# Optimization experiments

Measured on AMD Instinct MI355X. Metric: run time of the kernel, lower is better.

Reference implementation:

```python
import jax, jax.numpy as jnp
import numpy as np

DMODEL = 1024
N_MAMBAS = 4
D_INNER = 2 * DMODEL          # expand = 2
D_STATE = 16                  # mamba_ssm default
D_CONV = 4                    # mamba_ssm default
DT_RANK = DMODEL // 16        # ceil(d_model/16) = 64


def setup_inputs() -> dict:
    key = jax.random.key(0)
    ks = jax.random.split(key, 8)
    B, L, n = 2, 4096, N_MAMBAS
    f32 = jnp.float32
    x = jax.random.normal(ks[0], (B, L, DMODEL), f32)
    in_w = jax.random.normal(ks[1], (n, 2 * D_INNER, DMODEL), f32) * 0.02
    conv_w = jax.random.normal(ks[2], (n, D_INNER, D_CONV), f32) * 0.1
    conv_b = jnp.zeros((n, D_INNER), f32)
    xproj_w = jax.random.normal(ks[3], (n, DT_RANK + 2 * D_STATE, D_INNER), f32) * 0.02
    dt_w = jax.random.normal(ks[4], (n, D_INNER, DT_RANK), f32) * 0.02
    # softplus-inverse of dt_init ~ 0.01 (mamba-style dt bias init)
    dt_b = jnp.log(jnp.expm1(jnp.full((n, D_INNER), 0.01, f32)))
    # S4D-real init: A_log = log(1..d_state)
    A_log = jnp.log(jnp.broadcast_to(jnp.arange(1, D_STATE + 1, dtype=f32), (n, D_INNER, D_STATE)))
    D_skip = jnp.ones((n, D_INNER), f32)
    out_w = jax.random.normal(ks[5], (n, DMODEL, D_INNER), f32) * 0.02
    return dict(x=x, in_w=in_w, conv_w=conv_w, conv_b=conv_b, xproj_w=xproj_w,
                dt_w=dt_w, dt_b=dt_b, A_log=A_log, D_skip=D_skip, out_w=out_w)


def _mamba(x, in_w, conv_w, conv_b, xproj_w, dt_w, dt_b, A_log, D_skip, out_w):
    # x: (B, Lc, D)
    Bb = x.shape[0]
    xz = jnp.einsum('bld,ed->ble', x, in_w)                 # (B, Lc, 2*D_INNER)
    xi, z = jnp.split(xz, 2, axis=-1)
    # causal depthwise conv over time
    xc = jnp.transpose(xi, (0, 2, 1))                       # (B, D_INNER, Lc)
    xc = jax.lax.conv_general_dilated(xc, conv_w[:, None, :], (1,),
                                      [(D_CONV - 1, 0)], feature_group_count=D_INNER)
    xi = jax.nn.silu(jnp.transpose(xc + conv_b[None, :, None], (0, 2, 1)))  # (B, Lc, D_INNER)
    proj = jnp.einsum('bld,ed->ble', xi, xproj_w)           # (B, Lc, DT_RANK + 2*D_STATE)
    dt = proj[..., :DT_RANK]
    Bm = proj[..., DT_RANK:DT_RANK + D_STATE]
    Cm = proj[..., DT_RANK + D_STATE:]
    dt = jax.nn.softplus(jnp.einsum('blr,dr->bld', dt, dt_w) + dt_b)  # (B, Lc, D_INNER)
    A = -jnp.exp(A_log)                                     # (D_INNER, D_STATE)

    def step(h, inp):
        dt_t, B_t, C_t, x_t = inp                           # (B,Di),(B,Ds),(B,Ds),(B,Di)
        dA = jnp.exp(dt_t[:, :, None] * A)                  # (B, Di, Ds)
        h = dA * h + dt_t[:, :, None] * B_t[:, None, :] * x_t[:, :, None]
        return h, jnp.einsum('bds,bs->bd', h, C_t)

    h0 = jnp.zeros((Bb, D_INNER, D_STATE), x.dtype)
    xs_t = (jnp.swapaxes(dt, 0, 1), jnp.swapaxes(Bm, 0, 1),
            jnp.swapaxes(Cm, 0, 1), jnp.swapaxes(xi, 0, 1))
    _, ys = jax.lax.scan(step, h0, xs_t)                    # (Lc, B, D_INNER)
    y = jnp.swapaxes(ys, 0, 1) + xi * D_skip                # (B, Lc, D_INNER)
    y = y * jax.nn.silu(z)
    return jnp.einsum('ble,de->bld', y, out_w)              # (B, Lc, D)


def reference(x, in_w, conv_w, conv_b, xproj_w, dt_w, dt_b, A_log, D_skip, out_w):
    B, L, D = x.shape
    n = N_MAMBAS
    # strided slices x[:, i::n] == reshape(B, L//n, n, D)[:, :, i]
    xs = jnp.transpose(x.reshape(B, L // n, n, D), (2, 0, 1, 3))   # (n, B, Lc, D)
    ys = jax.vmap(_mamba)(xs, in_w, conv_w, conv_b, xproj_w,
                          dt_w, dt_b, A_log, D_skip, out_w)        # (n, B, Lc, D)
    # torch.cat(dim=1) concatenates per-mamba outputs block-wise along seq
    return jnp.transpose(ys, (1, 0, 2, 3)).reshape(B, L, D)
```

## Files before the change

### kernel.cpp

```cpp
#include <hip/hip_runtime.h>
#include <math.h>

#define DM   1024
#define DI   2048
#define DSn  16
#define DTR  64
#define PW   96
#define LS   1024
#define NCH  16
#define CL   64
#define XKS  8

typedef unsigned short u16;
typedef unsigned int   u32;
typedef __attribute__((ext_vector_type(8))) short bf16x8;
typedef __attribute__((ext_vector_type(8))) unsigned short u16x8;
typedef __attribute__((ext_vector_type(4))) float f32x4;

__device__ __forceinline__ void bar_lds() {
  asm volatile("s_waitcnt lgkmcnt(0)\n\ts_barrier" ::: "memory");
}

__device__ __forceinline__ void split2(float f, u16& hi, u16& lo) {
  union { float f; unsigned int u; } v; v.f = f;
  hi = (u16)(v.u >> 16);
  union { unsigned int u; float f; } w; w.u = v.u & 0xffff0000u;
  union { float f; unsigned int u; } r; r.f = f - w.f;
  lo = (u16)(r.u >> 16);
}

template<int ROWS>
__device__ __forceinline__ bf16x8 frag(const u16* T, int l4, int row) {
  return *(const bf16x8*)&T[(l4 * ROWS + row) * 8];
}

template<int ROWS>
__device__ __forceinline__ void stage16f(const float* a, u16* Th, u16* Tl, int ra, int half) {
  #pragma unroll
  for (int q = 0; q < 2; ++q) {
    u16x8 vh, vl;
    #pragma unroll
    for (int c = 0; c < 8; ++c) {
      u16 h_, l_;
      split2(a[q * 8 + c], h_, l_);
      vh[c] = h_; vl[c] = l_;
    }
    const int slot = ((half * 2 + q) * ROWS + ra) * 8;
    *(u16x8*)&Th[slot] = vh;
    *(u16x8*)&Tl[slot] = vl;
  }
}

__global__ __launch_bounds__(256) void k_split_x(
    const float* __restrict__ x, u16* __restrict__ xh, u16* __restrict__ xl, int ib0)
{
  const int idx = blockIdx.x * 256 + threadIdx.x;
  const int t = idx >> 8, kq = (idx & 255) * 4;
  const int gt = ib0 * 1024 + t;
  const int j = gt & (LS - 1), ib = gt >> 10;
  const int i = ib >> 1, bb = ib & 1;
  const float4 v = *(const float4*)&x[(size_t)(bb * 4096 + j * 4 + i) * DM + kq];
  ushort4 vh, vl;
  split2(v.x, vh.x, vl.x); split2(v.y, vh.y, vl.y);
  split2(v.z, vh.z, vl.z); split2(v.w, vh.w, vl.w);
  *(ushort4*)&xh[(size_t)t * DM + kq] = vh;
  *(ushort4*)&xl[(size_t)t * DM + kq] = vl;
}

#define KGP 2064
__global__ __launch_bounds__(512, 2) void k_inproj(
    const u16* __restrict__ xh, const u16* __restrict__ xl,
    const float* __restrict__ inwf,
    float* __restrict__ xz, int ib0, int swz)
{
  __shared__ __align__(16) u16 L[2][4][4][KGP];
  const int tid = threadIdx.x;
  int mblk, nblk;
  if (swz) {
    const int o = blockIdx.x;
    const int xcd = o & 7, within = o >> 3;
    mblk = xcd * 4 + (within & 3);
    nblk = within >> 2;
  } else {
    mblk = blockIdx.x; nblk = blockIdx.y;
  }
  const int m0 = mblk << 8, n0 = nblk << 8;
  const int ib = ib0 + (m0 >> 10);
  const int il = (ib >> 1) - (ib0 >> 1);
  const int ra = tid >> 1, half = tid & 1;
  const u16* Aph = xh + (size_t)(m0 + ra) * DM + half * 16;
  const u16* Apl = xl + (size_t)(m0 + ra) * DM + half * 16;
  const float* Bpf = inwf + ((size_t)il * 4096 + n0 + ra) * DM + half * 16;
  const int w = tid >> 6, lane = tid & 63;
  const int wr = w >> 2, wc = w & 3;
  const int l15 = lane & 15, l4 = lane >> 4;

  f32x4 acc[8][4];
  #pragma unroll
  for (int a_ = 0; a_ < 8; ++a_)
    #pragma unroll
    for (int b_ = 0; b_ < 4; ++b_) acc[a_][b_] = (f32x4)(0.f);

  u16x8 ah2[2], al2[2];
  float br[16];

  auto LOADG = [&](int kt) {
    const int k0 = kt * 32;
    ah2[0] = *(const u16x8*)(Aph + k0);
    ah2[1] = *(const u16x8*)(Aph + k0 + 8);
    al2[0] = *(const u16x8*)(Apl + k0);
    al2[1] = *(const u16x8*)(Apl + k0 + 8);
    *(f32x4*)&br[0]  = *(const f32x4*)(Bpf + k0);
    *(f32x4*)&br[4]  = *(const f32x4*)(Bpf + k0 + 4);
    *(f32x4*)&br[8]  = *(const f32x4*)(Bpf + k0 + 8);
    *(f32x4*)&br[12] = *(const f32x4*)(Bpf + k0 + 12);
  };
  auto STORE = [&](int b) {
    #pragma unroll
    for (int q = 0; q < 2; ++q) {
      const int kg = half * 2 + q;
      *(u16x8*)&L[b][0][kg][ra * 8] = ah2[q];
      *(u16x8*)&L[b][1][kg][ra * 8] = al2[q];
      u16x8 vh, vl;
      #pragma unroll
      for (int c = 0; c < 8; ++c) {
        u16 h_, l_;
        split2(br[q * 8 + c], h_, l_);
        vh[c] = h_; vl[c] = l_;
      }
      *(u16x8*)&L[b][2][kg][ra * 8] = vh;
      *(u16x8*)&L[b][3][kg][ra * 8] = vl;
    }
  };
  auto COMPUTE = [&](int b) {
    bf16x8 bh[4], bl[4];
    #pragma unroll
    for (int nf = 0; nf < 4; ++nf) {
      const int col = wc * 64 + nf * 16 + l15;
      bh[nf] = *(const bf16x8*)&L[b][2][l4][col * 8];
      bl[nf] = *(const bf16x8*)&L[b][3][l4][col * 8];
    }
    #pragma unroll
    for (int mf = 0; mf < 8; ++mf) {
      const int row = wr * 128 + mf * 16 + l15;
      bf16x8 ah = *(const bf16x8*)&L[b][0][l4][row * 8];
      bf16x8 al = *(const bf16x8*)&L[b][1][l4][row * 8];
      #pragma unroll
      for (int nf = 0; nf < 4; ++nf) {
        acc[mf][nf] = __builtin_amdgcn_mfma_f32_16x16x32_bf16(ah, bh[nf], acc[mf][nf], 0, 0, 0);
        acc[mf][nf] = __builtin_amdgcn_mfma_f32_16x16x32_bf16(ah, bl[nf], acc[mf][nf], 0, 0, 0);
        acc[mf][nf] = __builtin_amdgcn_mfma_f32_16x16x32_bf16(al, bh[nf], acc[mf][nf], 0, 0, 0);
      }
    }
  };

  const int nk = DM / 32;
  LOADG(0);
  STORE(0);
  if (nk > 1) LOADG(1);
  bar_lds();
  for (int kt = 0; kt < nk; ++kt) {
    const int c = kt & 1;
    if (kt + 1 < nk) STORE(c ^ 1);
    if (kt + 2 < nk) LOADG(kt + 2);
    COMPUTE(c);
    bar_lds();
  }

  #pragma unroll
  for (int mf = 0; mf < 8; ++mf) {
    const int row = m0 + wr * 128 + mf * 16 + l4 * 4;
    #pragma unroll
    for (int nf = 0; nf < 4; ++nf) {
      const int col = n0 + wc * 64 + nf * 16 + l15;
      #pragma unroll
      for (int r = 0; r < 4; ++r)
        xz[(size_t)(row + r) * (2 * DI) + col] = acc[mf][nf][r];
    }
  }
}

__global__ __launch_bounds__(256) void k_conv(
    const float* __restrict__ xz, const float* __restrict__ convw,
    const float* __restrict__ convb, float* __restrict__ xib,
    int ib0, int ntok)
{
  const int idx = blockIdx.x * 256 + threadIdx.x;
  if (idx >= ntok * (DI / 4)) return;
  const int t = idx / (DI / 4);
  const int c = (idx - t * (DI / 4)) * 4;
  const int j = t & (LS - 1);
  const int i = (ib0 + (t >> 10)) >> 1;
  float4 acc = *(const float4*)&convb[(size_t)i * DI + c];
  float4 wt[4];
  #pragma unroll
  for (int q = 0; q < 4; ++q)
    wt[q] = *(const float4*)&convw[((size_t)i * DI + c + q) * 4];
  #pragma unroll
  for (int k = 0; k < 4; ++k) {
    const int j2 = j + k - 3;
    if (j2 >= 0) {
      const float4 v = *(const float4*)&xz[(size_t)(t + k - 3) * (2 * DI) + c];
      acc.x = fmaf(v.x, ((const float*)&wt[0])[k], acc.x);
      acc.y = fmaf(v.y, ((const float*)&wt[1])[k], acc.y);
      acc.z = fmaf(v.z, ((const float*)&wt[2])[k], acc.z);
      acc.w = fmaf(v.w, ((const float*)&wt[3])[k], acc.w);
    }
  }
  float4 o;
  o.x = acc.x / (1.f + __expf(-acc.x));
  o.y = acc.y / (1.f + __expf(-acc.y));
  o.z = acc.z / (1.f + __expf(-acc.z));
  o.w = acc.w / (1.f + __expf(-acc.w));
  *(float4*)&xib[(size_t)t * DI + c] = o;
}

__global__ __launch_bounds__(256) void k_xproj_part(
    const float* __restrict__ xif, const float* __restrict__ xwf,
    float* __restrict__ Pp, int ib0, int ntok)
{
  __shared__ __align__(16) u16 Ah[4*64*8], Al[4*64*8];
  __shared__ __align__(16) u16 Bh[4*96*8], Bl[4*96*8];
  const int tid = threadIdx.x;
  const int m0 = blockIdx.x << 6;
  const int ks = blockIdx.y;
  const int kbase = ks * (DI / XKS);
  const int ib = ib0 + (m0 >> 10);
  const int il = (ib >> 1) - (ib0 >> 1);
  const int ra = tid >> 1, half = tid & 1;
  const bool hasA = (tid < 128);
  const bool hasB = (tid < 192);
  const float* Apf = xif + (size_t)(m0 + ra) * DI + kbase + half * 16;
  const float* Bpf = xwf + ((size_t)il * PW + ra) * DI + kbase + half * 16;
  const int w = tid >> 6, lane = tid & 63;
  const int l15 = lane & 15, l4 = lane >> 4;

  f32x4 acc[6];
  #pragma unroll
  for (int b_ = 0; b_ < 6; ++b_) acc[b_] = (f32x4)(0.f);

  float ar[16], br[16];
  if (hasA) {
    #pragma unroll
    for (int q = 0; q < 4; ++q) *(f32x4*)&ar[q*4] = *(const f32x4*)(Apf + q*4);
  }
  if (hasB) {
    #pragma unroll
    for (int q = 0; q < 4; ++q) *(f32x4*)&br[q*4] = *(const f32x4*)(Bpf + q*4);
  }
  const int nk = (DI / XKS) / 32;
  for (int kt = 0; kt < nk; ++kt) {
    bar_lds();
    if (hasA) stage16f<64>(ar, Ah, Al, ra, half);
    if (hasB) stage16f<96>(br, Bh, Bl, ra, half);
    bar_lds();
    if (kt + 1 < nk) {
      const int k0 = (kt + 1) * 32;
      if (hasA) {
        #pragma unroll
        for (int q = 0; q < 4; ++q) *(f32x4*)&ar[q*4] = *(const f32x4*)(Apf + k0 + q*4);
      }
      if (hasB) {
        #pragma unroll
        for (int q = 0; q < 4; ++q) *(f32x4*)&br[q*4] = *(const f32x4*)(Bpf + k0 + q*4);
      }
    }
    const int arow = w * 16 + l15;
    bf16x8 ah = frag<64>(Ah, l4, arow);
    bf16x8 al = frag<64>(Al, l4, arow);
    #pragma unroll
    for (int nf = 0; nf < 6; ++nf) {
      const int col = nf * 16 + l15;
      bf16x8 bh = frag<96>(Bh, l4, col);
      bf16x8 bl = frag<96>(Bl, l4, col);
      acc[nf] = __builtin_amdgcn_mfma_f32_16x16x32_bf16(ah, bh, acc[nf], 0, 0, 0);
      acc[nf] = __builtin_amdgcn_mfma_f32_16x16x32_bf16(ah, bl, acc[nf], 0, 0, 0);
      acc[nf] = __builtin_amdgcn_mfma_f32_16x16x32_bf16(al, bh, acc[nf], 0, 0, 0);
    }
  }
  float* outp = Pp + (size_t)ks * ntok * PW;
  const int row = m0 + w * 16 + l4 * 4;
  #pragma unroll
  for (int nf = 0; nf < 6; ++nf) {
    const int col = nf * 16 + l15;
    #pragma unroll
    for (int r = 0; r < 4; ++r)
      outp[(size_t)(row + r) * PW + col] = acc[nf][r];
  }
}

__global__ __launch_bounds__(256) void k_xproj_red(
    const float* __restrict__ Pp, float* __restrict__ projb, int ntok)
{
  const int idx = blockIdx.x * 256 + threadIdx.x;
  if (idx >= ntok * PW) return;
  const size_t plane = (size_t)ntok * PW;
  float s = 0.f;
  #pragma unroll
  for (int ks = 0; ks < XKS; ++ks) s += Pp[(size_t)ks * plane + idx];
  projb[idx] = s;
}

__global__ __launch_bounds__(256) void k_dtproj(
    const float* __restrict__ proj, const float* __restrict__ dtw,
    const float* __restrict__ dtbias, float* __restrict__ dtout,
    int dstride, int ib0)
{
  __shared__ float As[16][132];
  __shared__ float Bs[16][132];
  const int tid = threadIdx.x;
  const int n0 = blockIdx.x << 7;
  const int m0 = blockIdx.y << 7;
  const int ib = ib0 + (m0 >> 10);
  const int i  = ib >> 1;
  const int ar = tid >> 2, kq = tid & 3;
  const float* A0 = proj + (size_t)(m0 + ar) * PW + kq * 4;
  const float* A1 = A0 + (size_t)64 * PW;
  const float* Wb = dtw + (size_t)i * DI * DTR;
  const float* B0 = Wb + (size_t)(n0 + ar) * DTR + kq * 4;
  const float* B1 = B0 + (size_t)64 * DTR;
  const int tx = tid & 15, ty = tid >> 4;
  float acc[8][8] = {};
  for (int kt = 0; kt < DTR / 16; ++kt) {
    const int k0 = kt * 16;
    float4 a0 = *(const float4*)(A0 + k0);
    float4 a1 = *(const float4*)(A1 + k0);
    float4 b0 = *(const float4*)(B0 + k0);
    float4 b1 = *(const float4*)(B1 + k0);
    __syncthreads();
    As[kq*4+0][ar] = a0.x; As[kq*4+1][ar] = a0.y; As[kq*4+2][ar] = a0.z; As[kq*4+3][ar] = a0.w;
    As[kq*4+0][ar+64] = a1.x; As[kq*4+1][ar+64] = a1.y; As[kq*4+2][ar+64] = a1.z; As[kq*4+3][ar+64] = a1.w;
    Bs[kq*4+0][ar] = b0.x; Bs[kq*4+1][ar] = b0.y; Bs[kq*4+2][ar] = b0.z; Bs[kq*4+3][ar] = b0.w;
    Bs[kq*4+0][ar+64] = b1.x; Bs[kq*4+1][ar+64] = b1.y; Bs[kq*4+2][ar+64] = b1.z; Bs[kq*4+3][ar+64] = b1.w;
    __syncthreads();
    #pragma unroll
    for (int k = 0; k < 16; ++k) {
      const float4 av0 = *(const float4*)&As[k][ty*8];
      const float4 av1 = *(const float4*)&As[k][ty*8+4];
      const float4 bv0 = *(const float4*)&Bs[k][tx*8];
      const float4 bv1 = *(const float4*)&Bs[k][tx*8+4];
      const float aa[8] = {av0.x,av0.y,av0.z,av0.w,av1.x,av1.y,av1.z,av1.w};
      const float bv[8] = {bv0.x,bv0.y,bv0.z,bv0.w,bv1.x,bv1.y,bv1.z,bv1.w};
      #pragma unroll
      for (int r = 0; r < 8; ++r)
        #pragma unroll
        for (int c = 0; c < 8; ++c)
          acc[r][c] = fmaf(aa[r], bv[c], acc[r][c]);
    }
  }
  float bias[8];
  #pragma unroll
  for (int c = 0; c < 8; ++c) bias[c] = dtbias[(size_t)i * DI + n0 + tx*8 + c];
  #pragma unroll
  for (int r = 0; r < 8; ++r) {
    const int t = m0 + ty*8 + r;
    #pragma unroll
    for (int c = 0; c < 8; ++c) {
      float u = acc[r][c] + bias[c];
      float sp = (u > 20.f) ? u : log1pf(__expf(u));
      dtout[(size_t)t * dstride + n0 + tx*8 + c] = sp;
    }
  }
}

__global__ __launch_bounds__(256) void k_scan_part(
    const float* __restrict__ projb, const float* dtp, int dstride,
    const float* __restrict__ xib, const float* __restrict__ A_log,
    float* __restrict__ Pbuf, float* __restrict__ Hbuf, int ib0)
{
  const int d = blockIdx.x * 256 + threadIdx.x;
  const int ch = blockIdx.y, lib = blockIdx.z;
  const int i = (ib0 + lib) >> 1;
  const size_t gd = (size_t)i * DI + d;
  __shared__ float bs[CL][DSn];
  const size_t trow = (size_t)lib * LS + (size_t)ch * CL;
  for (int p = threadIdx.x; p < CL * DSn; p += 256) {
    const int jj = p >> 4, ss = p & 15;
    bs[jj][ss] = projb[(trow + jj) * PW + DTR + ss];
  }
  float A[DSn], P[DSn], h[DSn];
  #pragma unroll
  for (int s = 0; s < DSn; ++s) {
    A[s] = -__expf(A_log[gd * DSn + s]);
    P[s] = 1.f; h[s] = 0.f;
  }
  __syncthreads();
  float dt_c = dtp[trow * dstride + d];
  float xi_c = xib[trow * DI + d];
  for (int j = 0; j < CL; ++j) {
    float dt_n = 0.f, xi_n = 0.f;
    if (j + 1 < CL) {
      dt_n = dtp[(trow + j + 1) * dstride + d];
      xi_n = xib[(trow + j + 1) * DI + d];
    }
    const float dx = dt_c * xi_c;
    #pragma unroll
    for (int s = 0; s < DSn; ++s) {
      const float dA = __expf(dt_c * A[s]);
      P[s] *= dA;
      h[s] = fmaf(dA, h[s], dx * bs[j][s]);
    }
    dt_c = dt_n; xi_c = xi_n;
  }
  const size_t base = ((size_t)(lib * NCH + ch) * DSn) * DI + d;
  #pragma unroll
  for (int s = 0; s < DSn; ++s) {
    Pbuf[base + (size_t)s * DI] = P[s];
    Hbuf[base + (size_t)s * DI] = h[s];
  }
}

__global__ __launch_bounds__(256) void k_scan_mid(
    float* __restrict__ Pbuf, const float* __restrict__ Hbuf, int nib)
{
  const int idx = blockIdx.x * 256 + threadIdx.x;
  if (idx >= nib * DSn * DI) return;
  const int d = idx & (DI - 1);
  const int s = (idx >> 11) & 15;
  const int lib = idx >> 15;
  const size_t stride = (size_t)DSn * DI;
  const size_t base = ((size_t)lib * NCH * DSn + s) * DI + d;
  float carry = 0.f;
  for (int c = 0; c < NCH; ++c) {
    const size_t o = base + (size_t)c * stride;
    const float p = Pbuf[o];
    const float hl = Hbuf[o];
    Pbuf[o] = carry;
    carry = fmaf(p, carry, hl);
  }
}

__global__ __launch_bounds__(256) void k_scan_full(
    const float* __restrict__ projb, const float* dtp, int dstride,
    float* xibio, const float* xzz,
    const float* __restrict__ A_log, const float* __restrict__ D_skip,
    const float* __restrict__ Pbuf, int ib0)
{
  const int d = blockIdx.x * 256 + threadIdx.x;
  const int ch = blockIdx.y, lib = blockIdx.z;
  const int i = (ib0 + lib) >> 1;
  const size_t gd = (size_t)i * DI + d;
  __shared__ float bs[CL][2 * DSn];
  const size_t trow = (size_t)lib * LS + (size_t)ch * CL;
  for (int p = threadIdx.x; p < CL * 2 * DSn; p += 256) {
    const int jj = p >> 5, ss = p & 31;
    bs[jj][ss] = projb[(trow + jj) * PW + DTR + ss];
  }
  float A[DSn], h[DSn];
  const size_t hbase = ((size_t)(lib * NCH + ch) * DSn) * DI + d;
  #pragma unroll
  for (int s = 0; s < DSn; ++s) {
    A[s] = -__expf(A_log[gd * DSn + s]);
    h[s] = Pbuf[hbase + (size_t)s * DI];
  }
  const float Dsk = D_skip[gd];
  __syncthreads();
  float dt_c = dtp[trow * dstride + d];
  float xi_c = xibio[trow * DI + d];
  float z_c  = xzz[trow * (2 * DI) + DI + d];
  for (int j = 0; j < CL; ++j) {
    float dt_n = 0.f, xi_n = 0.f, z_n = 0.f;
    if (j + 1 < CL) {
      dt_n = dtp[(trow + j + 1) * dstride + d];
      xi_n = xibio[(trow + j + 1) * DI + d];
      z_n  = xzz[(trow + j + 1) * (2 * DI) + DI + d];
    }
    const float dx = dt_c * xi_c;
    float y = 0.f;
    #pragma unroll
    for (int s = 0; s < DSn; ++s) {
      const float dA = __expf(dt_c * A[s]);
      h[s] = fmaf(dA, h[s], dx * bs[j][s]);
      y = fmaf(h[s], bs[j][DSn + s], y);
    }
    const float sz = z_c / (1.f + __expf(-z_c));
    const float val = (y + xi_c * Dsk) * sz;
    u16 vh, vl;
    split2(val, vh, vl);
    ((u32*)xibio)[(trow + j) * DI + d] = ((u32)vh << 16) | (u32)vl;
    dt_c = dt_n; xi_c = xi_n; z_c = z_n;
  }
}

__global__ __launch_bounds__(256) void k_outproj(
    const u32* __restrict__ ybp, const float* __restrict__ owf,
    float* __restrict__ out, int ib0)
{
  __shared__ __align__(16) u16 Ah[4*128*8], Al[4*128*8];
  __shared__ __align__(16) u16 Bh[4*128*8], Bl[4*128*8];
  const int tid = threadIdx.x;
  const int m0 = blockIdx.x << 7;
  const int n0 = blockIdx.y << 7;
  const int ib = ib0 + (m0 >> 10);
  const int i = ib >> 1, bb = ib & 1;
  const int il = i - (ib0 >> 1);
  const int ra = tid >> 1, half = tid & 1;
  const u32* Ap = ybp + (size_t)(m0 + ra) * DI + half * 16;
  const int rb = tid >> 1;
  const float* Bpf = owf + ((size_t)il * DM + n0 + rb) * DI + half * 16;
  const int w = tid >> 6, lane = tid & 63;
  const int wr = w >> 1, wc = w & 1;
  const int l15 = lane & 15, l4 = lane >> 4;

  f32x4 acc[4][4];
  #pragma unroll
  for (int a_ = 0; a_ < 4; ++a_)
    #pragma unroll
    for (int b_ = 0; b_ < 4; ++b_) acc[a_][b_] = (f32x4)(0.f);

  uint4 qa[4];
  float br[16];
  qa[0] = *(const uint4*)(Ap);     qa[1] = *(const uint4*)(Ap + 4);
  qa[2] = *(const uint4*)(Ap + 8); qa[3] = *(const uint4*)(Ap + 12);
  #pragma unroll
  for (int q = 0; q < 4; ++q) *(f32x4*)&br[q*4] = *(const f32x4*)(Bpf + q*4);
  const int nk = DI / 32;
  for (int kt = 0; kt < nk; ++kt) {
    bar_lds();
    #pragma unroll
    for (int g = 0; g < 2; ++g) {
      const u32 e[8] = { qa[2*g].x, qa[2*g].y, qa[2*g].z, qa[2*g].w,
                         qa[2*g+1].x, qa[2*g+1].y, qa[2*g+1].z, qa[2*g+1].w };
      u16x8 vh, vl;
      #pragma unroll
      for (int c = 0; c < 8; ++c) { vh[c] = (u16)(e[c] >> 16); vl[c] = (u16)(e[c] & 0xffffu); }
      const int slot = ((half*2+g)*128 + ra)*8;
      *(u16x8*)&Ah[slot] = vh;
      *(u16x8*)&Al[slot] = vl;
    }
    stage16f<128>(br, Bh, Bl, rb, half);
    bar_lds();
    if (kt + 1 < nk) {
      const int k0 = (kt + 1) * 32;
      qa[0] = *(const uint4*)(Ap + k0);     qa[1] = *(const uint4*)(Ap + k0 + 4);
      qa[2] = *(const uint4*)(Ap + k0 + 8); qa[3] = *(const uint4*)(Ap + k0 + 12);
      #pragma unroll
      for (int q = 0; q < 4; ++q) *(f32x4*)&br[q*4] = *(const f32x4*)(Bpf + k0 + q*4);
    }
    bf16x8 ah[4], al[4];
    #pragma unroll
    for (int mf = 0; mf < 4; ++mf) {
      const int row = wr * 64 + mf * 16 + l15;
      ah[mf] = frag<128>(Ah, l4, row);
      al[mf] = frag<128>(Al, l4, row);
    }
    #pragma unroll
    for (int nf = 0; nf < 4; ++nf) {
      const int col = wc * 64 + nf * 16 + l15;
      bf16x8 bh = frag<128>(Bh, l4, col);
      bf16x8 bl = frag<128>(Bl, l4, col);
      #pragma unroll
      for (int mf = 0; mf < 4; ++mf) {
        acc[mf][nf] = __builtin_amdgcn_mfma_f32_16x16x32_bf16(ah[mf], bh, acc[mf][nf], 0, 0, 0);
        acc[mf][nf] = __builtin_amdgcn_mfma_f32_16x16x32_bf16(ah[mf], bl, acc[mf][nf], 0, 0, 0);
        acc[mf][nf] = __builtin_amdgcn_mfma_f32_16x16x32_bf16(al[mf], bh, acc[mf][nf], 0, 0, 0);
      }
    }
  }
  #pragma unroll
  for (int mf = 0; mf < 4; ++mf) {
    const int t0 = m0 + wr * 64 + mf * 16 + l4 * 4;
    #pragma unroll
    for (int nf = 0; nf < 4; ++nf) {
      const int col = n0 + wc * 64 + nf * 16 + l15;
      #pragma unroll
      for (int r = 0; r < 4; ++r) {
        const int j = (t0 + r) & (LS - 1);
        out[(size_t)(bb * 4096 + i * 1024 + j) * DM + col] = acc[mf][nf][r];
      }
    }
  }
}

extern "C" void kernel_launch(void* const* d_in, const int* in_sizes, int n_in,
                              void* d_out, int out_size, void* d_ws, size_t ws_size,
                              hipStream_t stream) {
  (void)in_sizes; (void)n_in; (void)out_size;
  const float* x       = (const float*)d_in[0];
  const float* in_w    = (const float*)d_in[1];
  const float* conv_w  = (const float*)d_in[2];
  const float* conv_b  = (const float*)d_in[3];
  const float* xproj_w = (const float*)d_in[4];
  const float* dt_w    = (const float*)d_in[5];
  const float* dt_b    = (const float*)d_in[6];
  const float* A_log   = (const float*)d_in[7];
  const float* D_skip  = (const float*)d_in[8];
  const float* out_w   = (const float*)d_in[9];
  float* out = (float*)d_out;
  const dim3 blk(256);

  const size_t needSP = ((size_t)8192 * 4096 + (size_t)8192 * 2048 + (size_t)8192 * 96) * 4;
  if (ws_size >= needSP) {
    const size_t nt = 8192;
    float* xz    = (float*)d_ws;
    float* xib   = xz + nt * (2 * DI);
    float* projb = xib + nt * DI;
    u16* xph  = (u16*)d_out;  u16* xpl  = xph + nt * DM;
    float* Pp = (float*)d_out;
    float* Pbuf = (float*)d_out;
    float* Hbuf = Pbuf + (size_t)8 * NCH * DSn * DI;
    float* dtz = xz;
    u32* ybp  = (u32*)xib;

    k_split_x<<<dim3((int)nt), blk, 0, stream>>>(x, xph, xpl, 0);
    k_inproj<<<dim3(512), dim3(512), 0, stream>>>(xph, xpl, in_w, xz, 0, 1);
    k_conv<<<dim3((int)(nt*(DI/4)/256)), blk, 0, stream>>>(xz, conv_w, conv_b, xib, 0, (int)nt);
    k_xproj_part<<<dim3((int)(nt/64), XKS), blk, 0, stream>>>(xib, xproj_w, Pp, 0, (int)nt);
    k_xproj_red<<<dim3((int)(nt*PW/256)), blk, 0, stream>>>(Pp, projb, (int)nt);
    k_dtproj<<<dim3(DI/128, (int)(nt/128)), blk, 0, stream>>>(projb, dt_w, dt_b, dtz, 2*DI, 0);
    k_scan_part<<<dim3(DI/256, NCH, 8), blk, 0, stream>>>(projb, dtz, 2*DI, xib, A_log, Pbuf, Hbuf, 0);
    k_scan_mid<<<dim3(8 * DSn * DI / 256), blk, 0, stream>>>(Pbuf, Hbuf, 8);
    k_scan_full<<<dim3(DI/256, NCH, 8), blk, 0, stream>>>(projb, dtz, 2*DI, xib, xz, A_log, D_skip, Pbuf, 0);
    k_outproj<<<dim3((int)(nt/128), 8), blk, 0, stream>>>(ybp, out_w, out, 0);
    return;
  }

  auto needFB = [](int nib) -> size_t { return (size_t)nib * 29753344ull; };
  const int step = (ws_size >= needFB(4)) ? 4 : 2;

  for (int ib0 = 0; ib0 < 8; ib0 += step) {
    const int nib = step;
    const size_t nt = (size_t)nib * LS;
    const int i0 = ib0 >> 1;
    float* xz    = (float*)d_ws;
    float* xib   = xz + nt * (2 * DI);
    float* projb = xib + nt * DI;
    float* SH    = projb + nt * PW;
    u16* xph  = (u16*)SH;  u16* xpl = xph + nt * DM;
    float* Pp = SH;
    float* Pbuf = SH;
    float* Hbuf = Pbuf + (size_t)nib * NCH * DSn * DI / 2;
    float* dtz = xz;
    u32* ybp  = (u32*)xib;

    k_split_x<<<dim3((int)nt), blk, 0, stream>>>(x, xph, xpl, ib0);
    k_inproj<<<dim3((int)(nt/256), 16), dim3(512), 0, stream>>>(xph, xpl, in_w + (size_t)i0*4096*DM, xz, ib0, 0);
    k_conv<<<dim3((int)(nt*(DI/4)/256)), blk, 0, stream>>>(xz, conv_w, conv_b, xib, ib0, (int)nt);
    k_xproj_part<<<dim3((int)(nt/64), XKS), blk, 0, stream>>>(xib, xproj_w + (size_t)i0*PW*DI, Pp, ib0, (int)nt);
    k_xproj_red<<<dim3((int)(nt*PW/256)), blk, 0, stream>>>(Pp, projb, (int)nt);
    k_dtproj<<<dim3(DI/128, (int)(nt/128)), blk, 0, stream>>>(projb, dt_w, dt_b, dtz, 2*DI, ib0);
    k_scan_part<<<dim3(DI/256, NCH, nib), blk, 0, stream>>>(projb, dtz, 2*DI, xib, A_log, Pbuf, Hbuf, ib0);
    k_scan_mid<<<dim3(nib * DSn * DI / 256), blk, 0, stream>>>(Pbuf, Hbuf, nib);
    k_scan_full<<<dim3(DI/256, NCH, nib), blk, 0, stream>>>(projb, dtz, 2*DI, xib, xz, A_log, D_skip, Pbuf, ib0);
    k_outproj<<<dim3((int)(nt/128), 8), blk, 0, stream>>>(ybp, out_w + (size_t)i0*DM*DI, out, ib0);
  }
}
```

Baseline: 634.0 us.

## Interleave LDS writes and global prefetch with MFMA clusters in in_proj GEMM

Splits the in_proj GEMM main loop into four MFMA clusters per k-tile, with two row-fragment pairs each. The staging of the next tile (A writes, B split-and-write, global prefetch of the tile after) is spread between these clusters. Each cluster is bracketed by barriers, a sched_barrier and s_setprio so that memory work and matrix math from different waves overlap. The loop is unrolled by two over the double buffers. The goal is to hide LDS store and global load latency behind MFMA issue, at the cost of many more barriers per k-tile.

New measurement: 654.8 us. +3.3%, slower.

```diff
diff --git a/kernel.cpp b/kernel.cpp
--- a/kernel.cpp
+++ b/kernel.cpp
@@ -104,68 +104,109 @@
   u16x8 ah2[2], al2[2];
   float br[16];
 
-  auto LOADG = [&](int kt) {
+  auto LOADA = [&](int kt) {
     const int k0 = kt * 32;
     ah2[0] = *(const u16x8*)(Aph + k0);
     ah2[1] = *(const u16x8*)(Aph + k0 + 8);
     al2[0] = *(const u16x8*)(Apl + k0);
     al2[1] = *(const u16x8*)(Apl + k0 + 8);
+  };
+  auto LOADB = [&](int kt) {
+    const int k0 = kt * 32;
     *(f32x4*)&br[0]  = *(const f32x4*)(Bpf + k0);
     *(f32x4*)&br[4]  = *(const f32x4*)(Bpf + k0 + 4);
     *(f32x4*)&br[8]  = *(const f32x4*)(Bpf + k0 + 8);
     *(f32x4*)&br[12] = *(const f32x4*)(Bpf + k0 + 12);
   };
-  auto STORE = [&](int b) {
-    #pragma unroll
-    for (int q = 0; q < 2; ++q) {
-      const int kg = half * 2 + q;
-      *(u16x8*)&L[b][0][kg][ra * 8] = ah2[q];
-      *(u16x8*)&L[b][1][kg][ra * 8] = al2[q];
-      u16x8 vh, vl;
-      #pragma unroll
-      for (int c = 0; c < 8; ++c) {
-        u16 h_, l_;
-        split2(br[q * 8 + c], h_, l_);
-        vh[c] = h_; vl[c] = l_;
-      }
-      *(u16x8*)&L[b][2][kg][ra * 8] = vh;
-      *(u16x8*)&L[b][3][kg][ra * 8] = vl;
-    }
+  auto WRA = [&](int b, int q) {
+    *(u16x8*)&L[b][0][half * 2 + q][ra * 8] = ah2[q];
+    *(u16x8*)&L[b][1][half * 2 + q][ra * 8] = al2[q];
   };
-  auto COMPUTE = [&](int b) {
-    bf16x8 bh[4], bl[4];
-    #pragma unroll
-    for (int nf = 0; nf < 4; ++nf) {
-      const int col = wc * 64 + nf * 16 + l15;
-      bh[nf] = *(const bf16x8*)&L[b][2][l4][col * 8];
-      bl[nf] = *(const bf16x8*)&L[b][3][l4][col * 8];
-    }
-    #pragma unroll
-    for (int mf = 0; mf < 8; ++mf) {
-      const int row = wr * 128 + mf * 16 + l15;
-      bf16x8 ah = *(const bf16x8*)&L[b][0][l4][row * 8];
-      bf16x8 al = *(const bf16x8*)&L[b][1][l4][row * 8];
-      #pragma unroll
-      for (int nf = 0; nf < 4; ++nf) {
-        acc[mf][nf] = __builtin_amdgcn_mfma_f32_16x16x32_bf16(ah, bh[nf], acc[mf][nf], 0, 0, 0);
-        acc[mf][nf] = __builtin_amdgcn_mfma_f32_16x16x32_bf16(ah, bl[nf], acc[mf][nf], 0, 0, 0);
-        acc[mf][nf] = __builtin_amdgcn_mfma_f32_16x16x32_bf16(al, bh[nf], acc[mf][nf], 0, 0, 0);
-      }
-    }
+  auto WRB = [&](int b, int q) {
+    u16x8 vh, vl;
+    #pragma unroll
+    for (int c = 0; c < 8; ++c) {
+      u16 h_, l_;
+      split2(br[q * 8 + c], h_, l_);
+      vh[c] = h_; vl[c] = l_;
+    }
+    *(u16x8*)&L[b][2][half * 2 + q][ra * 8] = vh;
+    *(u16x8*)&L[b][3][half * 2 + q][ra * 8] = vl;
   };
 
   const int nk = DM / 32;
-  LOADG(0);
-  STORE(0);
-  if (nk > 1) LOADG(1);
-  bar_lds();
-  for (int kt = 0; kt < nk; ++kt) {
-    const int c = kt & 1;
-    if (kt + 1 < nk) STORE(c ^ 1);
-    if (kt + 2 < nk) LOADG(kt + 2);
-    COMPUTE(c);
-    bar_lds();
-  }
+
+#define FENCE() do { \
+    __builtin_amdgcn_s_barrier(); \
+    asm volatile("s_waitcnt lgkmcnt(0)" ::: "memory"); \
+    __builtin_amdgcn_sched_barrier(0); \
+    __builtin_amdgcn_s_setprio(1); \
+  } while (0)
+#define ENDP() do { \
+    __builtin_amdgcn_s_setprio(0); \
+    __builtin_amdgcn_s_barrier(); \
+  } while (0)
+
+#define RD(C, PL, ROW) (*(const bf16x8*)&L[C][PL][l4][(ROW) * 8])
+
+#define CLUST(MB, A0H, A0L, A1H, A1L) do { \
+    _Pragma("unroll") \
+    for (int nf = 0; nf < 4; ++nf) { \
+      acc[MB][nf]   = __builtin_amdgcn_mfma_f32_16x16x32_bf16(A0H, bh[nf], acc[MB][nf], 0, 0, 0); \
+      acc[MB][nf]   = __builtin_amdgcn_mfma_f32_16x16x32_bf16(A0H, bl[nf], acc[MB][nf], 0, 0, 0); \
+      acc[MB][nf]   = __builtin_amdgcn_mfma_f32_16x16x32_bf16(A0L, bh[nf], acc[MB][nf], 0, 0, 0); \
+      acc[MB+1][nf] = __builtin_amdgcn_mfma_f32_16x16x32_bf16(A1H, bh[nf], acc[MB+1][nf], 0, 0, 0); \
+      acc[MB+1][nf] = __builtin_amdgcn_mfma_f32_16x16x32_bf16(A1H, bl[nf], acc[MB+1][nf], 0, 0, 0); \
+      acc[MB+1][nf] = __builtin_amdgcn_mfma_f32_16x16x32_bf16(A1L, bh[nf], acc[MB+1][nf], 0, 0, 0); \
+    } \
+  } while (0)
+
+#define TILE(C, KT) do { \
+    bf16x8 bh[4], bl[4]; \
+    bf16x8 a0h, a0l, a1h, a1l; \
+     \
+    _Pragma("unroll") \
+    for (int nf = 0; nf < 4; ++nf) { \
+      const int col = wc * 64 + nf * 16 + l15; \
+      bh[nf] = RD(C, 2, col); bl[nf] = RD(C, 3, col); \
+    } \
+    a0h = RD(C, 0, wr * 128 + 0 * 16 + l15);  a0l = RD(C, 1, wr * 128 + 0 * 16 + l15); \
+    a1h = RD(C, 0, wr * 128 + 1 * 16 + l15);  a1l = RD(C, 1, wr * 128 + 1 * 16 + l15); \
+    if ((KT) + 1 < nk) WRA((C) ^ 1, 0); \
+    FENCE(); CLUST(0, a0h, a0l, a1h, a1l); ENDP(); \
+     \
+    a0h = RD(C, 0, wr * 128 + 2 * 16 + l15);  a0l = RD(C, 1, wr * 128 + 2 * 16 + l15); \
+    a1h = RD(C, 0, wr * 128 + 3 * 16 + l15);  a1l = RD(C, 1, wr * 128 + 3 * 16 + l15); \
+    if ((KT) + 1 < nk) WRA((C) ^ 1, 1); \
+    FENCE(); CLUST(2, a0h, a0l, a1h, a1l); ENDP(); \
+     \
+    a0h = RD(C, 0, wr * 128 + 4 * 16 + l15);  a0l = RD(C, 1, wr * 128 + 4 * 16 + l15); \
+    a1h = RD(C, 0, wr * 128 + 5 * 16 + l15);  a1l = RD(C, 1, wr * 128 + 5 * 16 + l15); \
+    if ((KT) + 1 < nk) WRB((C) ^ 1, 0); \
+    if ((KT) + 2 < nk) LOADA((KT) + 2); \
+    FENCE(); CLUST(4, a0h, a0l, a1h, a1l); ENDP(); \
+     \
+    a0h = RD(C, 0, wr * 128 + 6 * 16 + l15);  a0l = RD(C, 1, wr * 128 + 6 * 16 + l15); \
+    a1h = RD(C, 0, wr * 128 + 7 * 16 + l15);  a1l = RD(C, 1, wr * 128 + 7 * 16 + l15); \
+    if ((KT) + 1 < nk) WRB((C) ^ 1, 1); \
+    if ((KT) + 2 < nk) LOADB((KT) + 2); \
+    FENCE(); CLUST(6, a0h, a0l, a1h, a1l); ENDP(); \
+  } while (0)
+
+  LOADA(0); LOADB(0);
+  WRA(0, 0); WRA(0, 1); WRB(0, 0); WRB(0, 1);
+  LOADA(1); LOADB(1);
+  __syncthreads();
+
+  for (int kt = 0; kt < nk; kt += 2) {
+    TILE(0, kt);
+    TILE(1, kt + 1);
+  }
+#undef TILE
+#undef CLUST
+#undef RD
+#undef FENCE
+#undef ENDP
 
   #pragma unroll
   for (int mf = 0; mf < 8; ++mf) {
```

## Double-buffer LDS tiles in xproj and outproj GEMM main loops

Applied to the files above, without the earlier changes.

Both the x-projection and out-projection GEMM kernels now use two LDS buffers. The next tile is staged into the alternate buffer while MFMA runs on the current one, and global loads are issued two tiles ahead. This removes one of the two barriers per k-iteration and lets LDS writes overlap compute. In exchange, LDS usage per block doubles (about 32KB for outproj), which may lower occupancy.

New measurement: 626.3 us. About the same (-1.2%).

```diff
diff --git a/kernel.cpp b/kernel.cpp
--- a/kernel.cpp
+++ b/kernel.cpp
@@ -219,8 +219,8 @@
     const float* __restrict__ xif, const float* __restrict__ xwf,
     float* __restrict__ Pp, int ib0, int ntok)
 {
-  __shared__ __align__(16) u16 Ah[4*64*8], Al[4*64*8];
-  __shared__ __align__(16) u16 Bh[4*96*8], Bl[4*96*8];
+  __shared__ __align__(16) u16 Ah[2][4*64*8], Al[2][4*64*8];
+  __shared__ __align__(16) u16 Bh[2][4*96*8], Bl[2][4*96*8];
   const int tid = threadIdx.x;
   const int m0 = blockIdx.x << 6;
   const int ks = blockIdx.y;
@@ -240,44 +240,49 @@
   for (int b_ = 0; b_ < 6; ++b_) acc[b_] = (f32x4)(0.f);
 
   float ar[16], br[16];
-  if (hasA) {
-    #pragma unroll
-    for (int q = 0; q < 4; ++q) *(f32x4*)&ar[q*4] = *(const f32x4*)(Apf + q*4);
-  }
-  if (hasB) {
-    #pragma unroll
-    for (int q = 0; q < 4; ++q) *(f32x4*)&br[q*4] = *(const f32x4*)(Bpf + q*4);
-  }
-  const int nk = (DI / XKS) / 32;
-  for (int kt = 0; kt < nk; ++kt) {
-    bar_lds();
-    if (hasA) stage16f<64>(ar, Ah, Al, ra, half);
-    if (hasB) stage16f<96>(br, Bh, Bl, ra, half);
-    bar_lds();
-    if (kt + 1 < nk) {
-      const int k0 = (kt + 1) * 32;
-      if (hasA) {
-        #pragma unroll
-        for (int q = 0; q < 4; ++q) *(f32x4*)&ar[q*4] = *(const f32x4*)(Apf + k0 + q*4);
-      }
-      if (hasB) {
-        #pragma unroll
-        for (int q = 0; q < 4; ++q) *(f32x4*)&br[q*4] = *(const f32x4*)(Bpf + k0 + q*4);
-      }
-    }
+  auto LOADAB = [&](int kt) {
+    const int k0 = kt * 32;
+    if (hasA) {
+      #pragma unroll
+      for (int q = 0; q < 4; ++q) *(f32x4*)&ar[q*4] = *(const f32x4*)(Apf + k0 + q*4);
+    }
+    if (hasB) {
+      #pragma unroll
+      for (int q = 0; q < 4; ++q) *(f32x4*)&br[q*4] = *(const f32x4*)(Bpf + k0 + q*4);
+    }
+  };
+  auto STORE = [&](int b) {
+    if (hasA) stage16f<64>(ar, Ah[b], Al[b], ra, half);
+    if (hasB) stage16f<96>(br, Bh[b], Bl[b], ra, half);
+  };
+  auto COMPUTE = [&](int b) {
     const int arow = w * 16 + l15;
-    bf16x8 ah = frag<64>(Ah, l4, arow);
-    bf16x8 al = frag<64>(Al, l4, arow);
+    bf16x8 ah = frag<64>(Ah[b], l4, arow);
+    bf16x8 al = frag<64>(Al[b], l4, arow);
     #pragma unroll
     for (int nf = 0; nf < 6; ++nf) {
       const int col = nf * 16 + l15;
-      bf16x8 bh = frag<96>(Bh, l4, col);
-      bf16x8 bl = frag<96>(Bl, l4, col);
+      bf16x8 bh = frag<96>(Bh[b], l4, col);
+      bf16x8 bl = frag<96>(Bl[b], l4, col);
       acc[nf] = __builtin_amdgcn_mfma_f32_16x16x32_bf16(ah, bh, acc[nf], 0, 0, 0);
       acc[nf] = __builtin_amdgcn_mfma_f32_16x16x32_bf16(ah, bl, acc[nf], 0, 0, 0);
       acc[nf] = __builtin_amdgcn_mfma_f32_16x16x32_bf16(al, bh, acc[nf], 0, 0, 0);
     }
-  }
+  };
+
+  const int nk = (DI / XKS) / 32;
+  LOADAB(0);
+  STORE(0);
+  LOADAB(1);
+  bar_lds();
+  for (int kt = 0; kt < nk; ++kt) {
+    const int c = kt & 1;
+    if (kt + 1 < nk) STORE(c ^ 1);
+    if (kt + 2 < nk) LOADAB(kt + 2);
+    COMPUTE(c);
+    bar_lds();
+  }
+
   float* outp = Pp + (size_t)ks * ntok * PW;
   const int row = m0 + w * 16 + l4 * 4;
   #pragma unroll
@@ -486,8 +491,8 @@
     const u32* __restrict__ ybp, const float* __restrict__ owf,
     float* __restrict__ out, int ib0)
 {
-  __shared__ __align__(16) u16 Ah[4*128*8], Al[4*128*8];
-  __shared__ __align__(16) u16 Bh[4*128*8], Bl[4*128*8];
+  __shared__ __align__(16) u16 Ah[2][4*128*8], Al[2][4*128*8];
+  __shared__ __align__(16) u16 Bh[2][4*128*8], Bl[2][4*128*8];
   const int tid = threadIdx.x;
   const int m0 = blockIdx.x << 7;
   const int n0 = blockIdx.y << 7;
@@ -510,13 +515,14 @@
 
   uint4 qa[4];
   float br[16];
-  qa[0] = *(const uint4*)(Ap);     qa[1] = *(const uint4*)(Ap + 4);
-  qa[2] = *(const uint4*)(Ap + 8); qa[3] = *(const uint4*)(Ap + 12);
-  #pragma unroll
-  for (int q = 0; q < 4; ++q) *(f32x4*)&br[q*4] = *(const f32x4*)(Bpf + q*4);
-  const int nk = DI / 32;
-  for (int kt = 0; kt < nk; ++kt) {
-    bar_lds();
+  auto LOADG = [&](int kt) {
+    const int k0 = kt * 32;
+    qa[0] = *(const uint4*)(Ap + k0);     qa[1] = *(const uint4*)(Ap + k0 + 4);
+    qa[2] = *(const uint4*)(Ap + k0 + 8); qa[3] = *(const uint4*)(Ap + k0 + 12);
+    #pragma unroll
+    for (int q = 0; q < 4; ++q) *(f32x4*)&br[q*4] = *(const f32x4*)(Bpf + k0 + q*4);
+  };
+  auto STORE = [&](int b) {
     #pragma unroll
     for (int g = 0; g < 2; ++g) {
       const u32 e[8] = { qa[2*g].x, qa[2*g].y, qa[2*g].z, qa[2*g].w,
@@ -525,30 +531,24 @@
       #pragma unroll
       for (int c = 0; c < 8; ++c) { vh[c] = (u16)(e[c] >> 16); vl[c] = (u16)(e[c] & 0xffffu); }
       const int slot = ((half*2+g)*128 + ra)*8;
-      *(u16x8*)&Ah[slot] = vh;
-      *(u16x8*)&Al[slot] = vl;
-    }
-    stage16f<128>(br, Bh, Bl, rb, half);
-    bar_lds();
-    if (kt + 1 < nk) {
-      const int k0 = (kt + 1) * 32;
-      qa[0] = *(const uint4*)(Ap + k0);     qa[1] = *(const uint4*)(Ap + k0 + 4);
-      qa[2] = *(const uint4*)(Ap + k0 + 8); qa[3] = *(const uint4*)(Ap + k0 + 12);
-      #pragma unroll
-      for (int q = 0; q < 4; ++q) *(f32x4*)&br[q*4] = *(const f32x4*)(Bpf + k0 + q*4);
-    }
+      *(u16x8*)&Ah[b][slot] = vh;
+      *(u16x8*)&Al[b][slot] = vl;
+    }
+    stage16f<128>(br, Bh[b], Bl[b], rb, half);
+  };
+  auto COMPUTE = [&](int b) {
     bf16x8 ah[4], al[4];
     #pragma unroll
     for (int mf = 0; mf < 4; ++mf) {
       const int row = wr * 64 + mf * 16 + l15;
-      ah[mf] = frag<128>(Ah, l4, row);
-      al[mf] = frag<128>(Al, l4, row);
+      ah[mf] = frag<128>(Ah[b], l4, row);
+      al[mf] = frag<128>(Al[b], l4, row);
     }
     #pragma unroll
     for (int nf = 0; nf < 4; ++nf) {
       const int col = wc * 64 + nf * 16 + l15;
-      bf16x8 bh = frag<128>(Bh, l4, col);
-      bf16x8 bl = frag<128>(Bl, l4, col);
+      bf16x8 bh = frag<128>(Bh[b], l4, col);
+      bf16x8 bl = frag<128>(Bl[b], l4, col);
       #pragma unroll
       for (int mf = 0; mf < 4; ++mf) {
         acc[mf][nf] = __builtin_amdgcn_mfma_f32_16x16x32_bf16(ah[mf], bh, acc[mf][nf], 0, 0, 0);
@@ -556,7 +556,21 @@
         acc[mf][nf] = __builtin_amdgcn_mfma_f32_16x16x32_bf16(al[mf], bh, acc[mf][nf], 0, 0, 0);
       }
     }
-  }
+  };
+
+  const int nk = DI / 32;
+  LOADG(0);
+  STORE(0);
+  LOADG(1);
+  bar_lds();
+  for (int kt = 0; kt < nk; ++kt) {
+    const int c = kt & 1;
+    if (kt + 1 < nk) STORE(c ^ 1);
+    if (kt + 2 < nk) LOADG(kt + 2);
+    COMPUTE(c);
+    bar_lds();
+  }
+
   #pragma unroll
   for (int mf = 0; mf < 4; ++mf) {
     const int t0 = m0 + wr * 64 + mf * 16 + l4 * 4;
```
